# Kernel tuning notes

Hardware: AMD Instinct MI355X
Metric: run time of the kernel (lower is better)

The kernel has to match this reference:

```python
import jax, jax.numpy as jnp
from jax import lax
import numpy as np

D_MODEL = 1024
D_STATE = 16
D_CONV = 4
EXPAND = 2
D_INNER = D_MODEL * EXPAND  # 2048
DT_RANK = (D_MODEL + 15) // 16  # 64
B_, L_ = 1, 1024


def setup_inputs() -> dict:
    key = jax.random.key(0)
    ks = jax.random.split(key, 14)
    f = lambda k, s, sc=0.02: (jax.random.normal(k, s, dtype=jnp.float32) * sc)
    A_log = jnp.log(jnp.tile(jnp.arange(1, D_STATE + 1, dtype=jnp.float32), (D_INNER, 1)))  # [d_inner, n]
    return {
        "x": jax.random.normal(ks[0], (B_, L_, D_MODEL), dtype=jnp.float32),
        "x1": jax.random.normal(ks[1], (B_, L_, D_MODEL), dtype=jnp.float32),
        "in_proj_w": f(ks[2], (2 * D_INNER, D_MODEL)),
        "in_proj1_w": f(ks[3], (D_INNER, D_MODEL)),
        "conv_w": f(ks[4], (D_INNER, 1, D_CONV), 0.1),
        "conv_b": f(ks[5], (D_INNER,), 0.1),
        "conv1_w": f(ks[6], (D_INNER, 1, D_CONV), 0.1),
        "conv1_b": f(ks[7], (D_INNER,), 0.1),
        "x_proj_w": f(ks[8], (DT_RANK + 2 * D_STATE, D_INNER)),
        "x_proj1_w": f(ks[9], (DT_RANK + 2 * D_STATE, D_INNER)),
        "dt_proj_w": f(ks[10], (D_INNER, DT_RANK), 0.1),
        "dt_proj1_w": f(ks[11], (D_INNER, DT_RANK), 0.1),
        "A_log": A_log,
        "A_log1": A_log,
        "Dskip": jnp.ones((D_INNER,), dtype=jnp.float32),
        "Dskip1": jnp.ones((D_INNER,), dtype=jnp.float32),
        "out_proj_w": f(ks[12], (D_MODEL, D_INNER)),
    }


def causal_conv1d_silu(x, w, b):
    # x: [b, d, l]; w: [d, 1, k] depthwise; left-pad (k-1) => causal
    y = lax.conv_general_dilated(
        x, w, window_strides=(1,), padding=[(D_CONV - 1, 0)],
        dimension_numbers=("NCW", "OIW", "NCW"), feature_group_count=D_INNER)
    return jax.nn.silu(y + b[None, :, None])


def selective_scan(u, delta, A, Bm, Cm, Dskip, z):
    # u, delta, z: [b, d, l]; A: [d, n]; Bm, Cm: [b, n, l]
    delta = jax.nn.softplus(delta)
    dd = jnp.moveaxis(delta, -1, 0)  # [l, b, d]
    du = jnp.moveaxis(u, -1, 0)      # [l, b, d]
    Bt = jnp.moveaxis(Bm, -1, 0)     # [l, b, n]
    Ct = jnp.moveaxis(Cm, -1, 0)     # [l, b, n]

    def step(h, inp):
        d_t, u_t, b_t, c_t = inp
        dA = jnp.exp(d_t[:, :, None] * A)                 # [b, d, n]
        dBu = (d_t * u_t)[:, :, None] * b_t[:, None, :]    # [b, d, n]
        h = dA * h + dBu
        y = jnp.einsum("bdn,bn->bd", h, c_t)
        return h, y

    b = u.shape[0]
    h0 = jnp.zeros((b, D_INNER, D_STATE), dtype=u.dtype)
    _, ys = lax.scan(step, h0, (dd, du, Bt, Ct))
    y = jnp.moveaxis(ys, 0, -1)  # [b, d, l]
    y = y + Dskip[None, :, None] * u
    return y * jax.nn.silu(z)


def reference(x, x1, in_proj_w, in_proj1_w, conv_w, conv_b, conv1_w, conv1_b,
              x_proj_w, x_proj1_w, dt_proj_w, dt_proj1_w, A_log, A_log1,
              Dskip, Dskip1, out_proj_w):
    # in-projections (no bias in original forward)
    xz = jnp.einsum("bld,ed->bel", x, in_proj_w)      # [b, 2*d_inner, l]
    x1p = jnp.einsum("bld,ed->bel", x1, in_proj1_w)   # [b, d_inner, l]
    xa, z = jnp.split(xz, 2, axis=1)
    A = -jnp.exp(A_log)
    A1 = -jnp.exp(A_log1)
    co = causal_conv1d_silu(xa, conv_w, conv_b)
    co1 = causal_conv1d_silu(x1p, conv1_w, conv1_b)

    def branch(co_b, xp_w, dt_w, A_b, D_b):
        x_dbl = jnp.einsum("bdl,kd->bkl", co_b, xp_w)            # [b, dt_rank+2n, l]
        delta = jnp.einsum("ek,bkl->bel", dt_w, x_dbl[:, :DT_RANK])  # no dt bias (delta_bias=None)
        Bm = x_dbl[:, DT_RANK:DT_RANK + D_STATE]
        Cm = x_dbl[:, DT_RANK + D_STATE:]
        return selective_scan(co_b, delta, A_b, Bm, Cm, D_b, z)  # z from branch-0 gates both

    out = branch(co, x_proj_w, dt_proj_w, A, Dskip)
    out1 = branch(co1, x_proj1_w, dt_proj1_w, A1, Dskip1)
    result = out + out1                                           # [b, d_inner, l]
    return jnp.einsum("bdl,ed->ble", result, out_proj_w)         # [b, l, d_model]
```

## Files before the change

kernel.cpp:

```cpp
#include <hip/hip_runtime.h>
#include <hip/hip_bf16.h>
#include <math.h>

#define D_MODEL 1024
#define D_STATE 16
#define D_CONV  4
#define D_INNER 2048
#define DT_RANK 64
#define LSEQ    1024

typedef short bf16x8 __attribute__((ext_vector_type(8)));
typedef float f32x4  __attribute__((ext_vector_type(4)));

__device__ __forceinline__ float softplus_f(float x) {
    const float sp = __logf(1.f + __expf(x));
    return (x > 20.f) ? x : sp;
}
__device__ __forceinline__ float silu_f(float x) {
    return x / (1.f + __expf(-x));
}
__device__ __forceinline__ unsigned short f2bf(float f) {
    union { float f; unsigned int u; } c; c.f = f;
    const unsigned int u = c.u;
    return (unsigned short)((u + 0x7FFFu + ((u >> 16) & 1u)) >> 16);
}

__global__ __launch_bounds__(256)
void cvt_all_k(const float* __restrict__ w0, const float* __restrict__ xx,
               const float* __restrict__ w1, const float* __restrict__ xx1,
               unsigned short* __restrict__ WB, unsigned short* __restrict__ XB,
               unsigned short* __restrict__ WB1, unsigned short* __restrict__ X1B)
{
    const int i = blockIdx.x * 256 + threadIdx.x;
    const float* src; unsigned short* dst; int j;
    if (i < (1 << 20))            { src = w0;  dst = WB;  j = i; }
    else if (i < (5 << 18))       { src = xx;  dst = XB;  j = i - (1 << 20); }
    else if (i < (7 << 18))       { src = w1;  dst = WB1; j = i - (5 << 18); }
    else                          { src = xx1; dst = X1B; j = i - (7 << 18); }
    const float4 v = *(const float4*)&src[(size_t)j * 4];
    ushort4 o;
    o.x = f2bf(v.x); o.y = f2bf(v.y); o.z = f2bf(v.z); o.w = f2bf(v.w);
    *(ushort4*)&dst[(size_t)j * 4] = o;
}

__global__ __launch_bounds__(256)
void cvt_k(const float* __restrict__ in, unsigned short* __restrict__ out, int n4)
{
    const int i = blockIdx.x * 256 + threadIdx.x;
    if (i >= n4) return;
    const float4 v = *(const float4*)&in[(size_t)i * 4];
    ushort4 o;
    o.x = f2bf(v.x); o.y = f2bf(v.y); o.z = f2bf(v.z); o.w = f2bf(v.w);
    *(ushort4*)&out[(size_t)i * 4] = o;
}

__global__ __launch_bounds__(256)
void cvtT_add_k(const float* __restrict__ r0, const float* __restrict__ r1,
                unsigned short* __restrict__ dst)
{
    __shared__ float s[32][33];
    const int tx = threadIdx.x & 31, ty = threadIdx.x >> 5;
    const int dBase = blockIdx.y * 32, lBase = blockIdx.x * 32;
    #pragma unroll
    for (int i = 0; i < 4; ++i) {
        const int d = dBase + ty + i * 8;
        const size_t off = (size_t)d * LSEQ + lBase + tx;
        s[ty + i * 8][tx] = r0[off] + r1[off];
    }
    __syncthreads();
    #pragma unroll
    for (int i = 0; i < 4; ++i) {
        const int l = lBase + ty + i * 8;
        dst[(size_t)l * D_INNER + dBase + tx] = f2bf(s[tx][ty + i * 8]);
    }
}

__device__ __forceinline__
void mfma_tile(const unsigned short* __restrict__ A, const unsigned short* __restrict__ B,
               float* __restrict__ C, int N, int K, int mBase, int nBase, int siluRow)
{
    __shared__ unsigned short As[128][40];
    __shared__ unsigned short Bs[128][40];
    const int tid = threadIdx.x;
    const int lane = tid & 63, w = tid >> 6;
    const int wr = w >> 1, wc = w & 1;
    const int l15 = lane & 15, l4 = lane >> 4;

    f32x4 acc[4][4] = {};
    const int sr = tid >> 2;
    const int sk = (tid & 3) * 8;

    for (int kb = 0; kb < K; kb += 32) {
        #pragma unroll
        for (int it = 0; it < 2; ++it) {
            const int r = it * 64 + sr;
            const float4 va = *(const float4*)&A[(size_t)(mBase + r) * K + kb + sk];
            *(float4*)&As[r][sk] = va;
            const float4 vb = *(const float4*)&B[(size_t)(nBase + r) * K + kb + sk];
            *(float4*)&Bs[r][sk] = vb;
        }
        __syncthreads();
        bf16x8 af[4], bfr[4];
        #pragma unroll
        for (int i = 0; i < 4; ++i) {
            af[i]  = *(const bf16x8*)&As[wr * 64 + i * 16 + l15][l4 * 8];
            bfr[i] = *(const bf16x8*)&Bs[wc * 64 + i * 16 + l15][l4 * 8];
        }
        #pragma unroll
        for (int i = 0; i < 4; ++i)
            #pragma unroll
            for (int j = 0; j < 4; ++j)
                acc[i][j] = __builtin_amdgcn_mfma_f32_16x16x32_bf16(af[i], bfr[j], acc[i][j], 0, 0, 0);
        __syncthreads();
    }

    #pragma unroll
    for (int i = 0; i < 4; ++i) {
        const int row0 = mBase + wr * 64 + i * 16 + l4 * 4;
        #pragma unroll
        for (int j = 0; j < 4; ++j) {
            const int col = nBase + wc * 64 + j * 16 + l15;
            #pragma unroll
            for (int r = 0; r < 4; ++r) {
                float v = acc[i][j][r];
                if (row0 + r >= siluRow) v = silu_f(v);
                C[(size_t)(row0 + r) * N + col] = v;
            }
        }
    }
}

__global__ __launch_bounds__(256)
void mfma_in_k(const unsigned short* __restrict__ WB, const unsigned short* __restrict__ XB,
               const unsigned short* __restrict__ WB1, const unsigned short* __restrict__ X1B,
               float* __restrict__ XZ, float* __restrict__ X1P)
{
    const int by = blockIdx.y;
    if (by < 32)
        mfma_tile(WB, XB, XZ, 1024, 1024, by * 128, blockIdx.x * 128, 2048);
    else
        mfma_tile(WB1, X1B, X1P, 1024, 1024, (by - 32) * 128, blockIdx.x * 128, 1 << 30);
}

__global__ __launch_bounds__(256)
void mfma_out_k(const unsigned short* __restrict__ RESTB, const unsigned short* __restrict__ OWB,
                float* __restrict__ C)
{
    mfma_tile(RESTB, OWB, C, 1024, 2048, blockIdx.y * 128, blockIdx.x * 128, 1 << 30);
}

constexpr int TS = 64;
constexpr int KT = 16;
constexpr int LP = 4;

__global__ __launch_bounds__(256)
void xproj_k(const float* __restrict__ xw0, const float* __restrict__ co0,
             const float* __restrict__ xw1, const float* __restrict__ co1,
             float* __restrict__ P0, float* __restrict__ P1)
{
    const int br = blockIdx.z >> 3;
    const int sl = blockIdx.z & 7;
    const float* A = (br ? xw1 : xw0) + sl * 256;
    const float* B = (br ? co1 : co0) + (size_t)sl * 256 * LSEQ;
    float* C = (br ? P1 : P0) + (size_t)sl * 96 * LSEQ;

    __shared__ float As[KT][TS + LP];
    __shared__ float Bs[KT][TS + LP];
    const int tid = threadIdx.x;
    const int tx = tid & 15, ty = tid >> 4;
    const int mBase = blockIdx.y * TS;
    const int nBase = blockIdx.x * TS;

    float acc[4][4] = {};
    const int ar = tid >> 2;
    const int ak = (tid & 3) * 4;

    for (int kb = 0; kb < 256; kb += KT) {
        {
            const int gm = mBase + ar;
            float4 av = make_float4(0.f, 0.f, 0.f, 0.f);
            if (gm < 96) av = *(const float4*)&A[(size_t)gm * D_INNER + kb + ak];
            As[ak + 0][ar] = av.x;
            As[ak + 1][ar] = av.y;
            As[ak + 2][ar] = av.z;
            As[ak + 3][ar] = av.w;
        }
        {
            const int bk = tid >> 4;
            const int bn = (tid & 15) * 4;
            const float4 bv = *(const float4*)&B[(size_t)(kb + bk) * LSEQ + nBase + bn];
            *(float4*)&Bs[bk][bn] = bv;
        }
        __syncthreads();
        #pragma unroll
        for (int k = 0; k < KT; ++k) {
            float4 a = *(const float4*)&As[k][ty * 4];
            float4 b = *(const float4*)&Bs[k][tx * 4];
            float av[4] = {a.x, a.y, a.z, a.w};
            float bv[4] = {b.x, b.y, b.z, b.w};
            #pragma unroll
            for (int i = 0; i < 4; ++i)
                #pragma unroll
                for (int j = 0; j < 4; ++j)
                    acc[i][j] = fmaf(av[i], bv[j], acc[i][j]);
        }
        __syncthreads();
    }

    #pragma unroll
    for (int i = 0; i < 4; ++i) {
        const int m = mBase + ty * 4 + i;
        if (m >= 96) continue;
        #pragma unroll
        for (int j = 0; j < 4; ++j)
            C[(size_t)m * LSEQ + nBase + tx * 4 + j] = acc[i][j];
    }
}

__global__ __launch_bounds__(256)
void reduceT_k(const float* __restrict__ P0, const float* __restrict__ P1,
               float* __restrict__ xdT0, float* __restrict__ xdT1)
{
    const int idx = blockIdx.x * 256 + threadIdx.x;
    const int k = idx & 127;
    const int l = (idx >> 7) & (LSEQ - 1);
    const int br = idx >> 17;
    if (k >= 96) return;
    const int srck = (k < 64) ? k : (64 + ((k - 64) >> 1) + ((k & 1) << 4));
    const float* P = br ? P1 : P0;
    float s = 0.f;
    #pragma unroll
    for (int sl = 0; sl < 8; ++sl)
        s += P[(size_t)sl * 96 * LSEQ + (size_t)srck * LSEQ + l];
    float* o = br ? xdT1 : xdT0;
    o[(size_t)l * 96 + k] = s;
}

__global__ __launch_bounds__(256)
void dtproj_k(const float* __restrict__ dtw0, const float* __restrict__ xdT0,
              const float* __restrict__ dtw1, const float* __restrict__ xdT1,
              float* __restrict__ SP0, float* __restrict__ SP1)
{
    const int br = blockIdx.z;
    const float* A = br ? dtw1 : dtw0;
    const float* B = br ? xdT1 : xdT0;
    float* C = br ? SP1 : SP0;

    __shared__ float As[KT][TS + LP];
    __shared__ float Bs[KT][TS + LP];
    const int tid = threadIdx.x;
    const int tx = tid & 15, ty = tid >> 4;
    const int mBase = blockIdx.y * TS;
    const int nBase = blockIdx.x * TS;

    float acc[4][4] = {};
    const int ar = tid >> 2;
    const int ak = (tid & 3) * 4;

    for (int kb = 0; kb < DT_RANK; kb += KT) {
        {
            const float4 av = *(const float4*)&A[(size_t)(mBase + ar) * DT_RANK + kb + ak];
            As[ak + 0][ar] = av.x;
            As[ak + 1][ar] = av.y;
            As[ak + 2][ar] = av.z;
            As[ak + 3][ar] = av.w;
        }
        {
            const float4 bv = *(const float4*)&B[(size_t)(nBase + ar) * 96 + kb + ak];
            Bs[ak + 0][ar] = bv.x;
            Bs[ak + 1][ar] = bv.y;
            Bs[ak + 2][ar] = bv.z;
            Bs[ak + 3][ar] = bv.w;
        }
        __syncthreads();
        #pragma unroll
        for (int k = 0; k < KT; ++k) {
            float4 a = *(const float4*)&As[k][ty * 4];
            float4 b = *(const float4*)&Bs[k][tx * 4];
            float av[4] = {a.x, a.y, a.z, a.w};
            float bv[4] = {b.x, b.y, b.z, b.w};
            #pragma unroll
            for (int i = 0; i < 4; ++i)
                #pragma unroll
                for (int j = 0; j < 4; ++j)
                    acc[i][j] = fmaf(av[i], bv[j], acc[i][j]);
        }
        __syncthreads();
    }

    #pragma unroll
    for (int i = 0; i < 4; ++i)
        #pragma unroll
        for (int j = 0; j < 4; ++j)
            C[(size_t)(mBase + ty * 4 + i) * LSEQ + nBase + tx * 4 + j] = softplus_f(acc[i][j]);
}

__global__ __launch_bounds__(256)
void conv_silu_k(const float* __restrict__ xa, const float* __restrict__ x1p,
                 const float* __restrict__ w0, const float* __restrict__ b0,
                 const float* __restrict__ w1, const float* __restrict__ b1,
                 float* __restrict__ co0, float* __restrict__ co1)
{
    const int idx = blockIdx.x * blockDim.x + threadIdx.x;
    const int br  = idx >> 21;
    const int rem = idx & ((1 << 21) - 1);
    const int d = rem >> 10;
    const int l = rem & (LSEQ - 1);

    const float* xin = br ? x1p : xa;
    const float* w   = br ? w1 : w0;
    const float* bb  = br ? b1 : b0;
    float* out       = br ? co1 : co0;

    const float* row = xin + (size_t)d * LSEQ;
    float acc = bb[d];
    #pragma unroll
    for (int j = 0; j < D_CONV; ++j) {
        const int li = l - (D_CONV - 1) + j;
        const float xv = (li >= 0) ? row[li] : 0.f;
        acc = fmaf(w[d * D_CONV + j], xv, acc);
    }
    out[rem] = silu_f(acc);
}

__global__ __launch_bounds__(512)
void scan7_k(const float* __restrict__ sp0, const float* __restrict__ u0,
             const float* __restrict__ xdT0,
             const float* __restrict__ Al0, const float* __restrict__ Dk0,
             const float* __restrict__ sp1, const float* __restrict__ u1,
             const float* __restrict__ xdT1,
             const float* __restrict__ Al1, const float* __restrict__ Dk1,
             const float* __restrict__ gz,
             float* __restrict__ res0, float* __restrict__ res1)
{
    const int d0  = blockIdx.x * 4;
    const int br  = blockIdx.y;
    const int tid = threadIdx.x;
    const int n   = tid & 15;
    const int c   = tid >> 4;

    const float* __restrict__ sp  = br ? sp1  : sp0;
    const float* __restrict__ u   = br ? u1   : u0;
    const float* __restrict__ xdT = br ? xdT1 : xdT0;
    const float* __restrict__ Al  = br ? Al1  : Al0;
    const float* __restrict__ Dk  = br ? Dk1  : Dk0;
    float* __restrict__ res       = br ? res1 : res0;

    float Adn[4], Dd[4];
    const float* srow[4]; const float* urow[4]; const float* grow[4]; float* orow[4];
    #pragma unroll
    for (int g = 0; g < 4; ++g) {
        Adn[g] = -__expf(Al[(d0 + g) * D_STATE + n]);
        Dd[g]  = Dk[d0 + g];
        srow[g] = sp + (size_t)(d0 + g) * LSEQ;
        urow[g] = u  + (size_t)(d0 + g) * LSEQ;
        grow[g] = gz + (size_t)(d0 + g) * LSEQ;
        orow[g] = res + (size_t)(d0 + g) * LSEQ;
    }
    const float* __restrict__ bc = xdT + 64 + 2 * n;
    const int t0 = c * 32;

    float a[4] = {1.f, 1.f, 1.f, 1.f};
    float b[4] = {0.f, 0.f, 0.f, 0.f};
    for (int tt = 0; tt < 32; tt += 4) {
        float2 bcv[4];
        #pragma unroll
        for (int j = 0; j < 4; ++j)
            bcv[j] = *(const float2*)&bc[(size_t)(t0 + tt + j) * 96];
        #pragma unroll
        for (int g = 0; g < 4; ++g) {
            const float4 s4 = *(const float4*)&srow[g][t0 + tt];
            const float4 u4 = *(const float4*)&urow[g][t0 + tt];
            const float sps[4] = {s4.x, s4.y, s4.z, s4.w};
            const float uvs[4] = {u4.x, u4.y, u4.z, u4.w};
            #pragma unroll
            for (int j = 0; j < 4; ++j) {
                const float dA = __expf(sps[j] * Adn[g]);
                a[g] *= dA;
                b[g] = fmaf(dA, b[g], sps[j] * uvs[j] * bcv[j].x);
            }
        }
    }

    __shared__ float sAm[32][16][4];
    __shared__ float sBm[32][16][4];
    __shared__ float sHm[32][16][4];
    #pragma unroll
    for (int g = 0; g < 4; ++g) { sAm[c][n][g] = a[g]; sBm[c][n][g] = b[g]; }
    __syncthreads();

    if (tid < 64) {
        const int n2 = tid & 15, g2 = tid >> 4;
        float hb = 0.f;
        #pragma unroll
        for (int cc = 0; cc < 32; ++cc) {
            sHm[cc][n2][g2] = hb;
            hb = fmaf(sAm[cc][n2][g2], hb, sBm[cc][n2][g2]);
        }
    }
    __syncthreads();

    float h[4];
    #pragma unroll
    for (int g = 0; g < 4; ++g) h[g] = sHm[c][n][g];

    for (int tt = 0; tt < 32; tt += 4) {
        float2 bcv[4];
        #pragma unroll
        for (int j = 0; j < 4; ++j)
            bcv[j] = *(const float2*)&bc[(size_t)(t0 + tt + j) * 96];
        #pragma unroll
        for (int g = 0; g < 4; ++g) {
            const float4 s4 = *(const float4*)&srow[g][t0 + tt];
            const float4 u4 = *(const float4*)&urow[g][t0 + tt];
            const float4 g4 = *(const float4*)&grow[g][t0 + tt];
            const float sps[4] = {s4.x, s4.y, s4.z, s4.w};
            const float uvs[4] = {u4.x, u4.y, u4.z, u4.w};
            const float gzs[4] = {g4.x, g4.y, g4.z, g4.w};
            float y4[4];
            #pragma unroll
            for (int j = 0; j < 4; ++j) {
                const float dA = __expf(sps[j] * Adn[g]);
                h[g] = fmaf(dA, h[g], sps[j] * uvs[j] * bcv[j].x);
                float y = h[g] * bcv[j].y;
                y += __shfl_xor(y, 1);
                y += __shfl_xor(y, 2);
                y += __shfl_xor(y, 4);
                y += __shfl_xor(y, 8);
                y4[j] = y;
            }
            if (n == 0) {
                float4 o;
                float* op = (float*)&o;
                #pragma unroll
                for (int j = 0; j < 4; ++j)
                    op[j] = (y4[j] + Dd[g] * uvs[j]) * gzs[j];
                *(float4*)&orow[g][t0 + tt] = o;
            }
        }
    }
}

extern "C" void kernel_launch(void* const* d_in, const int* in_sizes, int n_in,
                              void* d_out, int out_size, void* d_ws, size_t ws_size,
                              hipStream_t stream)
{
    const float* x          = (const float*)d_in[0];
    const float* x1         = (const float*)d_in[1];
    const float* in_proj_w  = (const float*)d_in[2];
    const float* in_proj1_w = (const float*)d_in[3];
    const float* conv_w     = (const float*)d_in[4];
    const float* conv_b     = (const float*)d_in[5];
    const float* conv1_w    = (const float*)d_in[6];
    const float* conv1_b    = (const float*)d_in[7];
    const float* x_proj_w   = (const float*)d_in[8];
    const float* x_proj1_w  = (const float*)d_in[9];
    const float* dt_proj_w  = (const float*)d_in[10];
    const float* dt_proj1_w = (const float*)d_in[11];
    const float* A_log      = (const float*)d_in[12];
    const float* A_log1     = (const float*)d_in[13];
    const float* Dskip      = (const float*)d_in[14];
    const float* Dskip1     = (const float*)d_in[15];
    const float* out_proj_w = (const float*)d_in[16];

    float* ws = (float*)d_ws;
    const size_t CH = (size_t)D_INNER * LSEQ;
    const size_t XD = (size_t)96 * LSEQ;
    const size_t F  = 5 * CH + 2 * XD;

    float* XA    = ws;
    float* RES0  = ws;
    float* GZ    = ws + CH;
    float* X1P   = ws + 2 * CH;
    float* RES1  = ws + 2 * CH;
    float* CO0   = ws + 3 * CH;
    float* CO1   = ws + 4 * CH;
    float* XDT0  = ws + 5 * CH;
    float* XDT1  = XDT0 + XD;
    float* XZ    = ws;

    unsigned short* WB  = (unsigned short*)(ws + F);
    unsigned short* XB  = (unsigned short*)(ws + F + 2097152);
    unsigned short* WB1 = (unsigned short*)(ws + F + 2097152 + 524288);
    unsigned short* X1B = (unsigned short*)(ws + F + 2097152 + 524288 + 1048576);
    float* P0  = ws + F;
    float* P1  = P0 + 8 * XD;
    float* SP0 = ws + F;
    float* SP1 = ws + F + CH;
    unsigned short* OWB   = (unsigned short*)(ws + F);
    unsigned short* RESTB = (unsigned short*)(ws + F + CH / 2);

    float* out = (float*)d_out;

    hipLaunchKernelGGL(cvt_all_k, dim3((2 << 20) / 256), dim3(256), 0, stream,
                       in_proj_w, x, in_proj1_w, x1, WB, XB, WB1, X1B);

    hipLaunchKernelGGL(mfma_in_k, dim3(8, 48), dim3(256), 0, stream,
                       WB, XB, WB1, X1B, XZ, X1P);

    hipLaunchKernelGGL(conv_silu_k, dim3(2 * D_INNER * LSEQ / 256), dim3(256), 0, stream,
                       XA, X1P, conv_w, conv_b, conv1_w, conv1_b, CO0, CO1);

    hipLaunchKernelGGL(xproj_k, dim3(LSEQ / TS, 2, 16), dim3(256), 0, stream,
                       x_proj_w, CO0, x_proj1_w, CO1, P0, P1);

    hipLaunchKernelGGL(reduceT_k, dim3(2 * LSEQ * 128 / 256), dim3(256), 0, stream,
                       P0, P1, XDT0, XDT1);

    hipLaunchKernelGGL(dtproj_k, dim3(LSEQ / TS, D_INNER / TS, 2), dim3(256), 0, stream,
                       dt_proj_w, XDT0, dt_proj1_w, XDT1, SP0, SP1);

    hipLaunchKernelGGL(scan7_k, dim3(D_INNER / 4, 2), dim3(512), 0, stream,
                       SP0, CO0, XDT0, A_log, Dskip,
                       SP1, CO1, XDT1, A_log1, Dskip1,
                       GZ, RES0, RES1);

    hipLaunchKernelGGL(cvt_k, dim3((1024 * 2048 / 4) / 256), dim3(256), 0, stream,
                       out_proj_w, OWB, 1024 * 2048 / 4);
    hipLaunchKernelGGL(cvtT_add_k, dim3(LSEQ / 32, D_INNER / 32), dim3(256), 0, stream,
                       RES0, RES1, RESTB);

    hipLaunchKernelGGL(mfma_out_k, dim3(8, 8), dim3(256), 0, stream,
                       RESTB, OWB, out);
}
```

Measured before the change: 236.6 us.

## Split-K the out-projection GEMM four ways with a separate reduction kernel

```diff
diff --git a/kernel.cpp b/kernel.cpp
--- a/kernel.cpp
+++ b/kernel.cpp
@@ -77,7 +77,7 @@
 
 __device__ __forceinline__
 void mfma_tile(const unsigned short* __restrict__ A, const unsigned short* __restrict__ B,
-               float* __restrict__ C, int N, int K, int mBase, int nBase, int siluRow)
+               float* __restrict__ C, int N, int K, int lda, int mBase, int nBase, int siluRow)
 {
     __shared__ unsigned short As[128][40];
     __shared__ unsigned short Bs[128][40];
@@ -94,9 +94,9 @@
         #pragma unroll
         for (int it = 0; it < 2; ++it) {
             const int r = it * 64 + sr;
-            const float4 va = *(const float4*)&A[(size_t)(mBase + r) * K + kb + sk];
+            const float4 va = *(const float4*)&A[(size_t)(mBase + r) * lda + kb + sk];
             *(float4*)&As[r][sk] = va;
-            const float4 vb = *(const float4*)&B[(size_t)(nBase + r) * K + kb + sk];
+            const float4 vb = *(const float4*)&B[(size_t)(nBase + r) * lda + kb + sk];
             *(float4*)&Bs[r][sk] = vb;
         }
         __syncthreads();
@@ -137,16 +137,32 @@
 {
     const int by = blockIdx.y;
     if (by < 32)
-        mfma_tile(WB, XB, XZ, 1024, 1024, by * 128, blockIdx.x * 128, 2048);
+        mfma_tile(WB, XB, XZ, 1024, 1024, 1024, by * 128, blockIdx.x * 128, 2048);
     else
-        mfma_tile(WB1, X1B, X1P, 1024, 1024, (by - 32) * 128, blockIdx.x * 128, 1 << 30);
+        mfma_tile(WB1, X1B, X1P, 1024, 1024, 1024, (by - 32) * 128, blockIdx.x * 128, 1 << 30);
 }
 
 __global__ __launch_bounds__(256)
 void mfma_out_k(const unsigned short* __restrict__ RESTB, const unsigned short* __restrict__ OWB,
-                float* __restrict__ C)
-{
-    mfma_tile(RESTB, OWB, C, 1024, 2048, blockIdx.y * 128, blockIdx.x * 128, 1 << 30);
+                float* __restrict__ P4)
+{
+    const int z = blockIdx.z;
+    mfma_tile(RESTB + z * 512, OWB + z * 512, P4 + (size_t)z * (1 << 20),
+              1024, 512, 2048, blockIdx.y * 128, blockIdx.x * 128, 1 << 30);
+}
+
+__global__ __launch_bounds__(256)
+void reduce4_k(const float* __restrict__ P, float* __restrict__ out)
+{
+    const int i = blockIdx.x * 256 + threadIdx.x;
+    const size_t o = (size_t)i * 4;
+    float4 s = *(const float4*)&P[o];
+    #pragma unroll
+    for (int z = 1; z < 4; ++z) {
+        const float4 v = *(const float4*)&P[(size_t)z * (1 << 20) + o];
+        s.x += v.x; s.y += v.y; s.z += v.z; s.w += v.w;
+    }
+    *(float4*)&out[o] = s;
 }
 
 constexpr int TS = 64;
@@ -475,6 +491,7 @@
     float* RES1  = ws + 2 * CH;
     float* CO0   = ws + 3 * CH;
     float* CO1   = ws + 4 * CH;
+    float* P4    = ws + 3 * CH;
     float* XDT0  = ws + 5 * CH;
     float* XDT1  = XDT0 + XD;
     float* XZ    = ws;
@@ -520,6 +537,8 @@
     hipLaunchKernelGGL(cvtT_add_k, dim3(LSEQ / 32, D_INNER / 32), dim3(256), 0, stream,
                        RES0, RES1, RESTB);
 
-    hipLaunchKernelGGL(mfma_out_k, dim3(8, 8), dim3(256), 0, stream,
-                       RESTB, OWB, out);
-}
+    hipLaunchKernelGGL(mfma_out_k, dim3(8, 8, 4), dim3(256), 0, stream,
+                       RESTB, OWB, P4);
+    hipLaunchKernelGGL(reduce4_k, dim3((1 << 18) / 256), dim3(256), 0, stream,
+                       P4, out);
+}
```

New measurement: 216.5 us. 1.09x faster.
